# Performance work log

Hardware: AMD Instinct MI355X
Metric: run time of the kernel (lower is better)

The kernel has to match this reference:

```python
import jax, jax.numpy as jnp
import numpy as np

MAX_TURNS = 11      # args.max_considered_history_turns
HIDDEN = 768        # args.bert_hidden
SEQ_LEN = 512       # max_seq_length
BATCH_SIZE = 64     # args.batch_size (== len(slice_mask))
SLICE_NUM = 16      # number of real examples in the batch
ROWS = 64           # sum of real slice_mask entries = rows of the inputs


def setup_inputs() -> dict:
    key = jax.random.key(0)
    k1, k2, k3, k4 = jax.random.split(key, 4)
    # 16 real examples with 4 history turns each (sum=64=ROWS); trailing 48
    # entries of 1 consume the zero-pad rows exactly as in the torch code.
    slice_mask = jnp.array([4] * SLICE_NUM + [1] * (BATCH_SIZE - SLICE_NUM),
                           dtype=jnp.int32)
    bert_representation = jax.random.normal(k1, (ROWS, SEQ_LEN, HIDDEN), jnp.float32)
    history_attention_input = jax.random.normal(k2, (ROWS, HIDDEN), jnp.float32)
    mtl_input = jax.random.normal(k3, (ROWS, HIDDEN), jnp.float32)
    W = 0.02 * jax.random.normal(k4, (1, HIDDEN), jnp.float32)  # linear weight, init std=0.02
    b = jnp.zeros((1,), jnp.float32)                            # linear bias
    return {
        "bert_representation": bert_representation,
        "history_attention_input": history_attention_input,
        "mtl_input": mtl_input,
        "W": W,
        "b": b,
        "slice_mask": slice_mask,
        "slice_num": SLICE_NUM,
    }


def reference(bert_representation, history_attention_input, mtl_input, W, b,
              slice_mask, slice_num):
    S = int(slice_num)
    T = MAX_TURNS
    rows = history_attention_input.shape[0]

    ns = slice_mask[:S]                                  # real turn counts [S]
    offsets = jnp.concatenate([jnp.zeros((1,), ns.dtype), jnp.cumsum(ns)[:-1]])
    pad_len = T - ns                                     # left zero-padding per example
    t = jnp.arange(T, dtype=ns.dtype)
    # gather index into the flat row axis for padded tensor [S, T]
    idx = offsets[:, None] + t[None, :] - pad_len[:, None]
    valid = (t[None, :] >= pad_len[:, None])             # sequence_mask flipped
    valid_f = valid.astype(history_attention_input.dtype)
    idx_c = jnp.clip(idx, 0, rows - 1)

    # padded history input [S, T, H]; invalid slots are zeros (ZeroPad2d)
    hist_pad = history_attention_input[idx_c] * valid_f[:, :, None]
    logits = jnp.einsum('sth,oh->st', hist_pad, W) + b[0]     # [S, T]
    exp_masked = jnp.exp(logits) * valid_f
    probs = exp_masked / jnp.sum(exp_masked, axis=1, keepdims=True)  # [S, T]

    # per-row weight: each real row r belongs to example seg[r] at turn tt[r]
    r = jnp.arange(rows)
    boundaries = jnp.cumsum(ns)
    seg = jnp.searchsorted(boundaries, r, side='right')       # [rows]
    pos = r - offsets[seg]
    tt = pad_len[seg] + pos
    w = probs[seg, tt]                                        # [rows]

    new_mtl_input = jax.ops.segment_sum(mtl_input * w[:, None], seg,
                                        num_segments=S)       # [S, H]
    new_bert_representation = jax.ops.segment_sum(
        bert_representation * w[:, None, None], seg, num_segments=S)  # [S, L, H]
    return new_bert_representation, new_mtl_input, probs
```

## Files before the change

kernel.cpp:

```cpp
#include <hip/hip_runtime.h>
#include <math.h>

#define T_MAX 11

__global__ __launch_bounds__(256) void k_fused(
    const float4* __restrict__ bert,
    const float4* __restrict__ mtl,
    const float*  __restrict__ hist,
    const float*  __restrict__ W,
    const float*  __restrict__ b,
    const int*    __restrict__ slice_mask,
    int S, int hidden,
    int bert_cols4, int mtl_cols4,
    int nchunks, int chunk_f4,
    float4* __restrict__ out_bert,
    float4* __restrict__ out_mtl,
    float*  __restrict__ out_probs)
{
    __shared__ float s_exp[T_MAX];
    __shared__ float s_wk[T_MAX];
    __shared__ int   s_off, s_n;

    const int sidx  = blockIdx.x / nchunks;
    const int chunk = blockIdx.x - sidx * nchunks;
    const int tid  = threadIdx.x;
    const int lane = tid & 63;
    const int wave = tid >> 6;

    if (tid == 0) {
        int acc = 0, n = 0;
        for (int i = 0; i < S; ++i) {
            const int v = slice_mask[i];
            if (i < sidx) acc += v;
            if (i == sidx) n = v;
        }
        s_off = acc;
        s_n   = n;
    }
    __syncthreads();

    const int o = s_off;
    const int n = s_n;

    for (int k = wave; k < n; k += 4) {
        const float* hrow = hist + (size_t)(o + k) * hidden;
        float acc = 0.0f;
        for (int h = lane; h < hidden; h += 64)
            acc += hrow[h] * W[h];
        #pragma unroll
        for (int d = 32; d > 0; d >>= 1)
            acc += __shfl_down(acc, d);
        if (lane == 0) s_exp[k] = expf(acc + b[0]);
    }
    __syncthreads();

    if (tid == 0) {
        float sum = 0.0f;
        for (int k = 0; k < n; ++k) sum += s_exp[k];
        const float inv = 1.0f / sum;
        for (int k = 0; k < n; ++k) s_wk[k] = s_exp[k] * inv;
    }
    __syncthreads();

    if (chunk == 0 && tid < T_MAX) {
        const int pad = T_MAX - n;
        out_probs[sidx * T_MAX + tid] = (tid >= pad) ? s_wk[tid - pad] : 0.0f;
    }

    const int total_f4 = bert_cols4 + mtl_cols4;
    const int lo = chunk * chunk_f4;
    const int hi = min(lo + chunk_f4, total_f4);

    for (int i = lo + tid; i < hi; i += 256) {
        float4 acc = {0.f, 0.f, 0.f, 0.f};
        if (i < bert_cols4) {
            const float4* p = bert + (size_t)o * bert_cols4 + i;
            for (int k = 0; k < n; ++k) {
                const float wk = s_wk[k];
                const float4 v = p[(size_t)k * bert_cols4];
                acc.x += wk * v.x; acc.y += wk * v.y;
                acc.z += wk * v.z; acc.w += wk * v.w;
            }
            out_bert[(size_t)sidx * bert_cols4 + i] = acc;
        } else {
            const int j = i - bert_cols4;
            const float4* p = mtl + (size_t)o * mtl_cols4 + j;
            for (int k = 0; k < n; ++k) {
                const float wk = s_wk[k];
                const float4 v = p[(size_t)k * mtl_cols4];
                acc.x += wk * v.x; acc.y += wk * v.y;
                acc.z += wk * v.z; acc.w += wk * v.w;
            }
            out_mtl[(size_t)sidx * mtl_cols4 + j] = acc;
        }
    }
}

extern "C" void kernel_launch(void* const* d_in, const int* in_sizes, int n_in,
                              void* d_out, int out_size, void* d_ws, size_t ws_size,
                              hipStream_t stream) {
    const float* bert = (const float*)d_in[0];
    const float* hist = (const float*)d_in[1];
    const float* mtl  = (const float*)d_in[2];
    const float* W    = (const float*)d_in[3];
    const float* b    = (const float*)d_in[4];
    const int* slice_mask = (const int*)d_in[5];

    const int hidden = in_sizes[3];
    const int rows   = in_sizes[1] / hidden;
    const int seq    = in_sizes[0] / (rows * hidden);
    const int S = out_size / (seq * hidden + hidden + T_MAX);

    float* out       = (float*)d_out;
    float* out_bert  = out;
    float* out_mtl   = out_bert + (size_t)S * seq * hidden;
    float* out_probs = out_mtl  + (size_t)S * hidden;

    const int bert_cols4 = seq * hidden / 4;
    const int mtl_cols4  = hidden / 4;
    const int total_f4   = bert_cols4 + mtl_cols4;

    const int chunk_f4 = 2048;
    const int nchunks  = (total_f4 + chunk_f4 - 1) / chunk_f4;
    const int grid     = S * nchunks;

    k_fused<<<grid, 256, 0, stream>>>((const float4*)bert, (const float4*)mtl,
                                      hist, W, b, slice_mask,
                                      S, hidden, bert_cols4, mtl_cols4,
                                      nchunks, chunk_f4,
                                      (float4*)out_bert, (float4*)out_mtl,
                                      out_probs);
}
```

Baseline: 172.6 us.

## Split softmax weights into separate kernel and restructure segment-sum with multi-accumulator loads

```diff
diff --git a/kernel.cpp b/kernel.cpp
--- a/kernel.cpp
+++ b/kernel.cpp
@@ -3,26 +3,22 @@
 
 #define T_MAX 11
 
-__global__ __launch_bounds__(256) void k_fused(
-    const float4* __restrict__ bert,
-    const float4* __restrict__ mtl,
-    const float*  __restrict__ hist,
-    const float*  __restrict__ W,
-    const float*  __restrict__ b,
-    const int*    __restrict__ slice_mask,
-    int S, int hidden,
-    int bert_cols4, int mtl_cols4,
-    int nchunks, int chunk_f4,
-    float4* __restrict__ out_bert,
-    float4* __restrict__ out_mtl,
-    float*  __restrict__ out_probs)
+__global__ __launch_bounds__(256) void k_probs(
+    const float* __restrict__ hist,
+    const float* __restrict__ W,
+    const float* __restrict__ b,
+    const int*   __restrict__ slice_mask,
+    int S, int rows, int hidden,
+    float* __restrict__ probs_out,
+    float* __restrict__ w_ws,
+    int*   __restrict__ ns_ws,
+    int*   __restrict__ off_ws)
 {
     __shared__ float s_exp[T_MAX];
     __shared__ float s_wk[T_MAX];
     __shared__ int   s_off, s_n;
 
-    const int sidx  = blockIdx.x / nchunks;
-    const int chunk = blockIdx.x - sidx * nchunks;
+    const int sidx = blockIdx.x;
     const int tid  = threadIdx.x;
     const int lane = tid & 63;
     const int wave = tid >> 6;
@@ -34,19 +30,25 @@
             if (i < sidx) acc += v;
             if (i == sidx) n = v;
         }
-        s_off = acc;
-        s_n   = n;
+        s_off = acc; s_n = n;
+        ns_ws[sidx] = n; off_ws[sidx] = acc;
     }
     __syncthreads();
 
     const int o = s_off;
     const int n = s_n;
+    const int h4 = hidden >> 2;
+    const float4* W4 = (const float4*)W;
 
     for (int k = wave; k < n; k += 4) {
-        const float* hrow = hist + (size_t)(o + k) * hidden;
+        int idx = min(o + k, rows - 1);
+        const float4* hrow = (const float4*)(hist + (size_t)idx * hidden);
         float acc = 0.0f;
-        for (int h = lane; h < hidden; h += 64)
-            acc += hrow[h] * W[h];
+        for (int j = lane; j < h4; j += 64) {
+            const float4 hv = hrow[j];
+            const float4 wv = W4[j];
+            acc += hv.x*wv.x + hv.y*wv.y + hv.z*wv.z + hv.w*wv.w;
+        }
         #pragma unroll
         for (int d = 32; d > 0; d >>= 1)
             acc += __shfl_down(acc, d);
@@ -58,40 +60,76 @@
         float sum = 0.0f;
         for (int k = 0; k < n; ++k) sum += s_exp[k];
         const float inv = 1.0f / sum;
-        for (int k = 0; k < n; ++k) s_wk[k] = s_exp[k] * inv;
+        for (int k = 0; k < n; ++k) {
+            const float wk = s_exp[k] * inv;
+            s_wk[k] = wk;
+            w_ws[o + k] = wk;
+        }
     }
     __syncthreads();
 
-    if (chunk == 0 && tid < T_MAX) {
+    if (tid < T_MAX) {
         const int pad = T_MAX - n;
-        out_probs[sidx * T_MAX + tid] = (tid >= pad) ? s_wk[tid - pad] : 0.0f;
+        probs_out[sidx * T_MAX + tid] = (tid >= pad) ? s_wk[tid - pad] : 0.0f;
+    }
+}
+
+__global__ __launch_bounds__(256) void k_segsum(
+    const float4* __restrict__ bert,
+    const float4* __restrict__ mtl,
+    const float*  __restrict__ w_ws,
+    const int*    __restrict__ ns_ws,
+    const int*    __restrict__ off_ws,
+    int nchunks, int bert_cols4, int mtl_cols4, int rows,
+    float4* __restrict__ out_bert,
+    float4* __restrict__ out_mtl)
+{
+    __shared__ float s_w[T_MAX];
+    __shared__ int   s_o, s_n;
+
+    const int sidx  = blockIdx.x / nchunks;
+    const int chunk = blockIdx.x - sidx * nchunks;
+    const int tid   = threadIdx.x;
+
+    if (tid == 0) { s_o = off_ws[sidx]; s_n = ns_ws[sidx]; }
+    __syncthreads();
+    if (tid < s_n) s_w[tid] = w_ws[s_o + tid];
+    __syncthreads();
+
+    const int o = s_o;
+    const int n = s_n;
+    const int total_f4 = bert_cols4 + mtl_cols4;
+    const int base = chunk * 1024 + tid;
+
+    float4 acc[4];
+    #pragma unroll
+    for (int j = 0; j < 4; ++j) acc[j] = make_float4(0.f, 0.f, 0.f, 0.f);
+
+    for (int k = 0; k < n; ++k) {
+        const float wk = s_w[k];
+        const int r = min(o + k, rows - 1);
+        const float4* brow = bert + (size_t)r * bert_cols4;
+        const float4* mrow = mtl  + (size_t)r * mtl_cols4;
+        #pragma unroll
+        for (int j = 0; j < 4; ++j) {
+            const int i = base + j * 256;
+            if (i < total_f4) {
+                const float4 v = (i < bert_cols4) ? brow[i]
+                                                  : mrow[i - bert_cols4];
+                acc[j].x += wk * v.x; acc[j].y += wk * v.y;
+                acc[j].z += wk * v.z; acc[j].w += wk * v.w;
+            }
+        }
     }
 
-    const int total_f4 = bert_cols4 + mtl_cols4;
-    const int lo = chunk * chunk_f4;
-    const int hi = min(lo + chunk_f4, total_f4);
-
-    for (int i = lo + tid; i < hi; i += 256) {
-        float4 acc = {0.f, 0.f, 0.f, 0.f};
-        if (i < bert_cols4) {
-            const float4* p = bert + (size_t)o * bert_cols4 + i;
-            for (int k = 0; k < n; ++k) {
-                const float wk = s_wk[k];
-                const float4 v = p[(size_t)k * bert_cols4];
-                acc.x += wk * v.x; acc.y += wk * v.y;
-                acc.z += wk * v.z; acc.w += wk * v.w;
-            }
-            out_bert[(size_t)sidx * bert_cols4 + i] = acc;
-        } else {
-            const int j = i - bert_cols4;
-            const float4* p = mtl + (size_t)o * mtl_cols4 + j;
-            for (int k = 0; k < n; ++k) {
-                const float wk = s_wk[k];
-                const float4 v = p[(size_t)k * mtl_cols4];
-                acc.x += wk * v.x; acc.y += wk * v.y;
-                acc.z += wk * v.z; acc.w += wk * v.w;
-            }
-            out_mtl[(size_t)sidx * mtl_cols4 + j] = acc;
+    #pragma unroll
+    for (int j = 0; j < 4; ++j) {
+        const int i = base + j * 256;
+        if (i < total_f4) {
+            if (i < bert_cols4)
+                out_bert[(size_t)sidx * bert_cols4 + i] = acc[j];
+            else
+                out_mtl[(size_t)sidx * mtl_cols4 + (i - bert_cols4)] = acc[j];
         }
     }
 }
@@ -116,18 +154,23 @@
     float* out_mtl   = out_bert + (size_t)S * seq * hidden;
     float* out_probs = out_mtl  + (size_t)S * hidden;
 
+    char*  wsb   = (char*)d_ws;
+    float* w_ws  = (float*)wsb;
+    size_t ofs   = (((size_t)rows * sizeof(float)) + 255) & ~(size_t)255;
+    int*   ns_ws  = (int*)(wsb + ofs);
+    int*   off_ws = ns_ws + S;
+
+    k_probs<<<S, 256, 0, stream>>>(hist, W, b, slice_mask, S, rows, hidden,
+                                   out_probs, w_ws, ns_ws, off_ws);
+
     const int bert_cols4 = seq * hidden / 4;
     const int mtl_cols4  = hidden / 4;
     const int total_f4   = bert_cols4 + mtl_cols4;
+    const int nchunks    = (total_f4 + 1023) / 1024;
+    const int grid       = S * nchunks;
 
-    const int chunk_f4 = 2048;
-    const int nchunks  = (total_f4 + chunk_f4 - 1) / chunk_f4;
-    const int grid     = S * nchunks;
-
-    k_fused<<<grid, 256, 0, stream>>>((const float4*)bert, (const float4*)mtl,
-                                      hist, W, b, slice_mask,
-                                      S, hidden, bert_cols4, mtl_cols4,
-                                      nchunks, chunk_f4,
-                                      (float4*)out_bert, (float4*)out_mtl,
-                                      out_probs);
+    k_segsum<<<grid, 256, 0, stream>>>((const float4*)bert, (const float4*)mtl,
+                                       w_ws, ns_ws, off_ws,
+                                       nchunks, bert_cols4, mtl_cols4, rows,
+                                       (float4*)out_bert, (float4*)out_mtl);
 }
```

Result: no change. 173.8 us (+0.7%).
